# Performance work log

Measured on AMD Instinct MI355X. Metric: run time of the kernel, lower is better.

## Reference

```python
import jax, jax.numpy as jnp
import numpy as np

NEG_INF = -1e9


def setup_inputs() -> dict:
    key = jax.random.key(0)
    ks = jax.random.split(key, 12)
    B, S, D, H = 32, 2048, 512, 512
    enc_outs = jax.random.normal(ks[0], (B, S, D), dtype=jnp.float32)
    num_sent = jnp.maximum(jax.random.randint(ks[1], (B,), 0, S), 1).astype(jnp.int64)
    s = 1.0 / np.sqrt(H)
    return {
        "enc_outs": enc_outs,
        "num_sent": num_sent,
        "num_pred": 8,
        "init_h": jax.random.normal(ks[2], (1, H), dtype=jnp.float32) * s,
        "init_c": jax.random.normal(ks[3], (1, H), dtype=jnp.float32) * s,
        "init_in": jax.random.normal(ks[4], (D,), dtype=jnp.float32) * s,
        "W_ih": jax.random.uniform(ks[5], (4 * H, D), jnp.float32, -s, s),
        "W_hh": jax.random.uniform(ks[6], (4 * H, H), jnp.float32, -s, s),
        "b_ih": jax.random.uniform(ks[7], (4 * H,), jnp.float32, -s, s),
        "b_hh": jax.random.uniform(ks[8], (4 * H,), jnp.float32, -s, s),
        "attn_Wq": jax.random.uniform(ks[9], (H, D), jnp.float32, -s, s),
        "score_W": jax.random.uniform(ks[10], (1, H), jnp.float32, -s, s),
        "score_b": jax.random.uniform(ks[11], (1,), jnp.float32, -s, s),
    }


def reference(enc_outs, num_sent, num_pred, init_h, init_c, init_in,
              W_ih, W_hh, b_ih, b_hh, attn_Wq, score_W, score_b):
    B, S, D = enc_outs.shape
    H = init_h.shape[1]
    # rep_mask: True where sentence index is valid
    mask = jnp.arange(S)[None, :] < num_sent[:, None]  # [B, S]

    def lstm_cell(x, h, c):
        gates = x @ W_ih.T + b_ih + h @ W_hh.T + b_hh  # [B, 4H]
        i, f, g, o = jnp.split(gates, 4, axis=-1)
        i, f, o = jax.nn.sigmoid(i), jax.nn.sigmoid(f), jax.nn.sigmoid(o)
        c_new = f * c + i * jnp.tanh(g)
        return o * jnp.tanh(c_new), c_new

    h0 = jnp.broadcast_to(init_h[0], (B, H))
    c0 = jnp.broadcast_to(init_c[0], (B, H))
    in0 = jnp.broadcast_to(init_in, (B, D))

    def step(carry, _):
        h, c, lstm_in = carry
        h, c = lstm_cell(lstm_in, h, c)
        # glimpse attention: bilinear score, masked softmax over sentences
        q = h @ attn_Wq  # [B, D]
        logits = jnp.einsum('bd,bsd->bs', q, enc_outs)
        logits = jnp.where(mask, logits, NEG_INF)
        attn = jax.nn.softmax(logits, axis=-1)
        out = jnp.einsum('bs,bsd->bd', attn, enc_outs)  # [B, D]
        score = out @ score_W.T + score_b  # [B, 1]
        return (h, c, out), score

    _, scores = jax.lax.scan(step, (h0, c0, in0), None, length=int(num_pred))
    return scores  # [num_pred, B, 1]
```

## Files before the change

### kernel.cpp

```cpp
#include <hip/hip_runtime.h>
#include <math.h>

#define B    32
#define S    2048
#define D    512
#define H    512
#define NP   8
#define NSL  32
#define HSL  16
#define NBT  8
#define BG   4
#define NCH  8
#define SCHUNK 256

__device__ __forceinline__ float sigmoidf_(float x) {
  return 1.0f / (1.0f + __expf(-x));
}

__global__ __launch_bounds__(256)
void k_init(const float* __restrict__ W_ih, const float* __restrict__ W_hh,
            const float* __restrict__ init_h, const float* __restrict__ init_c,
            const float* __restrict__ init_in, const int* __restrict__ ns_raw,
            float* __restrict__ Wt, float* __restrict__ hbuf, float* __restrict__ cbuf,
            float* __restrict__ xin0, int* __restrict__ ns) {
  __shared__ float tbuf[64][65];
  const int blk = blockIdx.x, tid = threadIdx.x;
  const int jt = blk & 31, kt = blk >> 5;
  const int j0 = jt * 64, k0 = kt * 64;
  const int r0 = tid >> 6, cc = tid & 63;
  for (int rr = r0; rr < 64; rr += 4) {
    int j = j0 + rr, k = k0 + cc;
    tbuf[rr][cc] = (k < 512) ? W_ih[(size_t)j * 512 + k]
                             : W_hh[(size_t)j * 512 + (k - 512)];
  }
  __syncthreads();
  for (int rr = r0; rr < 64; rr += 4)
    Wt[(size_t)(k0 + rr) * 2048 + j0 + cc] = tbuf[cc][rr];

  int idx = blk * 256 + tid;
  if (idx < B * H) {
    int d = idx & 511;
    hbuf[idx] = init_h[d];
    cbuf[idx] = init_c[d];
    xin0[idx] = init_in[d];
  }
  if (idx == 0) {
    bool is64 = (ns_raw[1] == 0);
    for (int i = 0; i < B; ++i) ns[i] = is64 ? ns_raw[2 * i] : ns_raw[i];
  }
}

__global__ __launch_bounds__(512, 1)
void k_step(const float* __restrict__ xin0, const float* __restrict__ bih,
            const float* __restrict__ bhh, const float* __restrict__ Wq,
            const float* __restrict__ scW, const float* __restrict__ scb,
            const float* __restrict__ Wt,
            const float* __restrict__ ch_m, const float* __restrict__ ch_l,
            const float* __restrict__ ch_o,
            float* __restrict__ hbuf, float* __restrict__ cbuf,
            float* __restrict__ qpart, float* __restrict__ out, int t) {
  __shared__ float X[BG][1024];
  __shared__ float gacc[8][64][5];
  __shared__ float gl[4][16][BG];
  __shared__ float hl[BG][16];
  __shared__ float sred[8][BG];

  const int tid = threadIdx.x;
  const int sl = blockIdx.x >> 3;
  const int bg = blockIdx.x & 7;
  const int b0 = bg * BG;

  if (t == 0) {
    #pragma unroll
    for (int bl = 0; bl < BG; ++bl)
      X[bl][tid] = xin0[(b0 + bl) * 512 + tid];
  } else {
    const float swd = scW[tid];
    #pragma unroll
    for (int bl = 0; bl < BG; ++bl) {
      const int b = b0 + bl;
      float M = -1e30f;
      #pragma unroll
      for (int c = 0; c < NCH; ++c) M = fmaxf(M, ch_m[b * NCH + c]);
      float e[NCH]; float L = 0.f;
      #pragma unroll
      for (int c = 0; c < NCH; ++c) {
        e[c] = __expf(ch_m[b * NCH + c] - M);
        L += ch_l[b * NCH + c] * e[c];
      }
      float v = 0.f;
      #pragma unroll
      for (int c = 0; c < NCH; ++c)
        v += ch_o[((size_t)(b * NCH + c)) * 512 + tid] * e[c];
      v *= (1.0f / L);
      X[bl][tid] = v;
      float p = v * swd;
      #pragma unroll
      for (int off = 32; off > 0; off >>= 1) p += __shfl_xor(p, off);
      if ((tid & 63) == 0) sred[tid >> 6][bl] = p;
    }
  }
  if (t < NP) {
    const float4* hsrc = (const float4*)(hbuf + (t & 1) * (B * 512));
    int bl = tid >> 7;
    int off = tid & 127;
    float4 hv = hsrc[(b0 + bl) * 128 + off];
    *(float4*)&X[bl][512 + off * 4] = hv;
  }
  __syncthreads();

  if (t >= 1 && tid < BG) {
    float s = 0.f;
    #pragma unroll
    for (int w = 0; w < 8; ++w) s += sred[w][tid];
    if (sl == 0) out[(t - 1) * B + b0 + tid] = s + scb[0];
  }
  if (t >= NP) return;

  {
    const int jloc = tid & 63;
    const int kc = tid >> 6;
    const int gi = jloc >> 4, ho = jloc & 15;
    const int jg = gi * 512 + sl * HSL + ho;
    const int k0c = kc * 128;
    const float* wp = Wt + (size_t)k0c * 2048 + jg;
    float acc[BG] = {0, 0, 0, 0};
    for (int kk = 0; kk < 32; ++kk) {
      float wv0 = wp[(size_t)(kk * 4 + 0) * 2048];
      float wv1 = wp[(size_t)(kk * 4 + 1) * 2048];
      float wv2 = wp[(size_t)(kk * 4 + 2) * 2048];
      float wv3 = wp[(size_t)(kk * 4 + 3) * 2048];
      #pragma unroll
      for (int bl = 0; bl < BG; ++bl) {
        const float4 xv = *(const float4*)&X[bl][k0c + kk * 4];
        acc[bl] += wv0 * xv.x + wv1 * xv.y + wv2 * xv.z + wv3 * xv.w;
      }
    }
    #pragma unroll
    for (int bl = 0; bl < BG; ++bl) gacc[kc][jloc][bl] = acc[bl];
  }
  __syncthreads();

  if (tid < 256) {
    const int bl = tid >> 6, jloc = tid & 63;
    const int gi = jloc >> 4, ho = jloc & 15;
    const int jg = gi * 512 + sl * HSL + ho;
    float g = bih[jg] + bhh[jg];
    #pragma unroll
    for (int kc = 0; kc < 8; ++kc) g += gacc[kc][jloc][bl];
    gl[gi][ho][bl] = g;
  }
  __syncthreads();

  if (tid < BG * HSL) {
    const int ho = tid & 15, bl = tid >> 4;
    const int bglob = b0 + bl, hid = sl * HSL + ho;
    float i_ = sigmoidf_(gl[0][ho][bl]);
    float f_ = sigmoidf_(gl[1][ho][bl]);
    float g_ = tanhf(gl[2][ho][bl]);
    float o_ = sigmoidf_(gl[3][ho][bl]);
    float cv = cbuf[bglob * 512 + hid];
    float cn = f_ * cv + i_ * g_;
    cbuf[bglob * 512 + hid] = cn;
    float hv = o_ * tanhf(cn);
    hbuf[((t + 1) & 1) * (B * 512) + bglob * 512 + hid] = hv;
    hl[bl][ho] = hv;
  }
  __syncthreads();

  {
    float w[HSL];
    #pragma unroll
    for (int ho = 0; ho < HSL; ++ho)
      w[ho] = Wq[(size_t)(sl * HSL + ho) * 512 + tid];
    #pragma unroll
    for (int bl = 0; bl < BG; ++bl) {
      float acc = 0.f;
      #pragma unroll
      for (int ho = 0; ho < HSL; ++ho) acc += hl[bl][ho] * w[ho];
      qpart[((size_t)sl * B + b0 + bl) * 512 + tid] = acc;
    }
  }
}

__global__ __launch_bounds__(512, 1)
void k_attn(const float* __restrict__ enc, const float* __restrict__ qpart,
            const int* __restrict__ ns_buf, float* __restrict__ ch_m,
            float* __restrict__ ch_l, float* __restrict__ ch_o) {
  __shared__ float q_lds[512];
  __shared__ float wm[8], wl[8];
  __shared__ float wo[8][512];
  const int b  = blockIdx.x >> 3;
  const int ch = blockIdx.x & 7;
  const int tid = threadIdx.x;
  const int lane = tid & 63;
  const int wv = tid >> 6;

  {
    float s = 0.f;
    #pragma unroll 8
    for (int sl = 0; sl < NSL; ++sl)
      s += qpart[((size_t)sl * B + b) * 512 + tid];
    q_lds[tid] = s;
  }
  __syncthreads();

  const float4 qa  = *(const float4*)&q_lds[lane * 8];
  const float4 qb4 = *(const float4*)&q_lds[lane * 8 + 4];

  const int s0 = ch * SCHUNK;
  const int nsb = ns_buf[b];
  float m = -1e30f, l = 0.f;
  float o0=0,o1=0,o2=0,o3=0,o4=0,o5=0,o6=0,o7=0;

  const int send = min(s0 + SCHUNK, nsb);
  const size_t rowbase = (size_t)b * S;

  int r = s0 + 2 * wv;
  if (r < send) {
    bool has1 = (r + 1 < send);
    const float4* p0 = (const float4*)(enc + (rowbase + r) * 512 + lane * 8);
    const float4* p1 = (const float4*)(enc + (rowbase + (has1 ? r + 1 : r)) * 512 + lane * 8);
    float4 a0 = p0[0], a1 = p0[1];
    float4 c0 = p1[0], c1 = p1[1];
    while (true) {
      const int rn = r + 16;
      const bool hasn = (rn < send);
      float4 na0, na1, nc0, nc1;
      bool nhas1 = false;
      if (hasn) {
        nhas1 = (rn + 1 < send);
        const float4* f0 = (const float4*)(enc + (rowbase + rn) * 512 + lane * 8);
        const float4* f1 = (const float4*)(enc + (rowbase + (nhas1 ? rn + 1 : rn)) * 512 + lane * 8);
        na0 = f0[0]; na1 = f0[1]; nc0 = f1[0]; nc1 = f1[1];
      }
      float d0 = qa.x*a0.x + qa.y*a0.y + qa.z*a0.z + qa.w*a0.w
               + qb4.x*a1.x + qb4.y*a1.y + qb4.z*a1.z + qb4.w*a1.w;
      float d1 = qa.x*c0.x + qa.y*c0.y + qa.z*c0.z + qa.w*c0.w
               + qb4.x*c1.x + qb4.y*c1.y + qb4.z*c1.z + qb4.w*c1.w;
      #pragma unroll
      for (int off = 32; off > 0; off >>= 1) {
        d0 += __shfl_xor(d0, off);
        d1 += __shfl_xor(d1, off);
      }
      if (!has1) d1 = -1e30f;
      float nm = fmaxf(m, fmaxf(d0, d1));
      float sc = __expf(m - nm);
      float w0 = __expf(d0 - nm);
      float w1 = __expf(d1 - nm);
      l = l * sc + w0 + w1;
      o0 = o0*sc + w0*a0.x + w1*c0.x; o1 = o1*sc + w0*a0.y + w1*c0.y;
      o2 = o2*sc + w0*a0.z + w1*c0.z; o3 = o3*sc + w0*a0.w + w1*c0.w;
      o4 = o4*sc + w0*a1.x + w1*c1.x; o5 = o5*sc + w0*a1.y + w1*c1.y;
      o6 = o6*sc + w0*a1.z + w1*c1.z; o7 = o7*sc + w0*a1.w + w1*c1.w;
      m = nm;
      if (!hasn) break;
      r = rn; has1 = nhas1;
      a0 = na0; a1 = na1; c0 = nc0; c1 = nc1;
    }
  }
  if (lane == 0) { wm[wv] = m; wl[wv] = l; }
  float4* wop = (float4*)&wo[wv][lane * 8];
  wop[0] = make_float4(o0, o1, o2, o3);
  wop[1] = make_float4(o4, o5, o6, o7);
  __syncthreads();

  float M = wm[0];
  #pragma unroll
  for (int w = 1; w < 8; ++w) M = fmaxf(M, wm[w]);
  float e[8]; float L = 0.f;
  #pragma unroll
  for (int w = 0; w < 8; ++w) { e[w] = __expf(wm[w] - M); L += wl[w] * e[w]; }
  if (tid == 0) { ch_m[b * NCH + ch] = M; ch_l[b * NCH + ch] = L; }
  float v = 0.f;
  #pragma unroll
  for (int w = 0; w < 8; ++w) v += wo[w][tid] * e[w];
  ch_o[((size_t)(b * NCH + ch)) * 512 + tid] = v;
}

extern "C" void kernel_launch(void* const* d_in, const int* in_sizes, int n_in,
                              void* d_out, int out_size, void* d_ws, size_t ws_size,
                              hipStream_t stream) {
  const float* enc     = (const float*)d_in[0];
  const int*   ns_raw  = (const int*)d_in[1];
  const float* init_h  = (const float*)d_in[3];
  const float* init_c  = (const float*)d_in[4];
  const float* init_in = (const float*)d_in[5];
  const float* W_ih    = (const float*)d_in[6];
  const float* W_hh    = (const float*)d_in[7];
  const float* b_ih    = (const float*)d_in[8];
  const float* b_hh    = (const float*)d_in[9];
  const float* Wq      = (const float*)d_in[10];
  const float* score_W = (const float*)d_in[11];
  const float* score_b = (const float*)d_in[12];
  float* out = (float*)d_out;

  float* ws    = (float*)d_ws;
  float* Wt    = ws;
  float* hbuf  = ws + 2097152;
  float* cbuf  = ws + 2129920;
  float* xin0  = ws + 2146304;
  float* qpart = ws + 2162688;
  float* ch_m  = ws + 2686976;
  float* ch_l  = ws + 2687232;
  float* ch_o  = ws + 2687488;
  int*   ns    = (int*)(ws + 2818560);

  k_init<<<512, 256, 0, stream>>>(W_ih, W_hh, init_h, init_c, init_in, ns_raw,
                                  Wt, hbuf, cbuf, xin0, ns);
  for (int t = 0; t < NP; ++t) {
    k_step<<<NSL * NBT, 512, 0, stream>>>(xin0, b_ih, b_hh, Wq, score_W, score_b, Wt,
                                          ch_m, ch_l, ch_o, hbuf, cbuf, qpart, out, t);
    k_attn<<<B * NCH, 512, 0, stream>>>(enc, qpart, ns, ch_m, ch_l, ch_o);
  }
  k_step<<<NSL * NBT, 512, 0, stream>>>(xin0, b_ih, b_hh, Wq, score_W, score_b, Wt,
                                        ch_m, ch_l, ch_o, hbuf, cbuf, qpart, out, NP);
}
```

Before: 309.6 us.

## Interleave 8-row groups across all waves to balance attention work per batch

The attention kernel now gives each wave interleaved groups of 8 consecutive sentence rows, strided by 64 groups across all chunk blocks of a batch row. Before, each block owned a fixed 256-row chunk, so for short sequences most blocks sat idle. This spreads the valid rows evenly and raises memory-level parallelism with 8-row double-buffered loads per wave. The cost is heavy register use: 32 float4 buffers per thread may hurt occupancy or spill. The last group may also read up to 7 padded rows past the valid length, which are masked out.

```diff
diff --git a/kernel.cpp b/kernel.cpp
--- a/kernel.cpp
+++ b/kernel.cpp
@@ -208,61 +208,82 @@
   const float4 qa  = *(const float4*)&q_lds[lane * 8];
   const float4 qb4 = *(const float4*)&q_lds[lane * 8 + 4];
 
-  const int s0 = ch * SCHUNK;
   const int nsb = ns_buf[b];
+  const int gid = ch * 8 + wv;
+  const size_t rowbase = (size_t)b * S;
+  const int ngroups = (nsb + 7) >> 3;
+  const int niter = (gid < ngroups) ? ((ngroups - gid + 63) >> 6) : 0;
+
   float m = -1e30f, l = 0.f;
-  float o0=0,o1=0,o2=0,o3=0,o4=0,o5=0,o6=0,o7=0;
-
-  const int send = min(s0 + SCHUNK, nsb);
-  const size_t rowbase = (size_t)b * S;
-
-  int r = s0 + 2 * wv;
-  if (r < send) {
-    bool has1 = (r + 1 < send);
-    const float4* p0 = (const float4*)(enc + (rowbase + r) * 512 + lane * 8);
-    const float4* p1 = (const float4*)(enc + (rowbase + (has1 ? r + 1 : r)) * 512 + lane * 8);
-    float4 a0 = p0[0], a1 = p0[1];
-    float4 c0 = p1[0], c1 = p1[1];
-    while (true) {
-      const int rn = r + 16;
-      const bool hasn = (rn < send);
-      float4 na0, na1, nc0, nc1;
-      bool nhas1 = false;
-      if (hasn) {
-        nhas1 = (rn + 1 < send);
-        const float4* f0 = (const float4*)(enc + (rowbase + rn) * 512 + lane * 8);
-        const float4* f1 = (const float4*)(enc + (rowbase + (nhas1 ? rn + 1 : rn)) * 512 + lane * 8);
-        na0 = f0[0]; na1 = f0[1]; nc0 = f1[0]; nc1 = f1[1];
-      }
-      float d0 = qa.x*a0.x + qa.y*a0.y + qa.z*a0.z + qa.w*a0.w
-               + qb4.x*a1.x + qb4.y*a1.y + qb4.z*a1.z + qb4.w*a1.w;
-      float d1 = qa.x*c0.x + qa.y*c0.y + qa.z*c0.z + qa.w*c0.w
-               + qb4.x*c1.x + qb4.y*c1.y + qb4.z*c1.z + qb4.w*c1.w;
+  float4 acc0 = make_float4(0,0,0,0), acc1 = make_float4(0,0,0,0);
+
+  float4 cx[8], cy[8], nx[8], ny[8];
+
+#define LOADG(g, X, Y)                                                        \
+  {                                                                           \
+    const size_t rb = rowbase + (size_t)(g) * 8;                              \
+    _Pragma("unroll")                                                         \
+    for (int j = 0; j < 8; ++j) {                                             \
+      const float4* p = (const float4*)(enc + (rb + j) * 512 + lane * 8);     \
+      X[j] = p[0]; Y[j] = p[1];                                               \
+    }                                                                         \
+  }
+
+  if (niter > 0) {
+    int g = gid;
+    LOADG(g, cx, cy);
+    for (int i = 0; i < niter; ++i) {
+      const bool has = (i + 1 < niter);
+      if (has) LOADG(g + 64, nx, ny);
+
+      float d[8];
+      #pragma unroll
+      for (int j = 0; j < 8; ++j)
+        d[j] = qa.x*cx[j].x + qa.y*cx[j].y + qa.z*cx[j].z + qa.w*cx[j].w
+             + qb4.x*cy[j].x + qb4.y*cy[j].y + qb4.z*cy[j].z + qb4.w*cy[j].w;
       #pragma unroll
       for (int off = 32; off > 0; off >>= 1) {
-        d0 += __shfl_xor(d0, off);
-        d1 += __shfl_xor(d1, off);
-      }
-      if (!has1) d1 = -1e30f;
-      float nm = fmaxf(m, fmaxf(d0, d1));
+        #pragma unroll
+        for (int j = 0; j < 8; ++j) d[j] += __shfl_xor(d[j], off);
+      }
+      const int rbase = g * 8;
+      #pragma unroll
+      for (int j = 0; j < 8; ++j)
+        if (rbase + j >= nsb) d[j] = -1e30f;
+
+      float gm = fmaxf(fmaxf(fmaxf(d[0], d[1]), fmaxf(d[2], d[3])),
+                       fmaxf(fmaxf(d[4], d[5]), fmaxf(d[6], d[7])));
+      float nm = fmaxf(m, gm);
       float sc = __expf(m - nm);
-      float w0 = __expf(d0 - nm);
-      float w1 = __expf(d1 - nm);
-      l = l * sc + w0 + w1;
-      o0 = o0*sc + w0*a0.x + w1*c0.x; o1 = o1*sc + w0*a0.y + w1*c0.y;
-      o2 = o2*sc + w0*a0.z + w1*c0.z; o3 = o3*sc + w0*a0.w + w1*c0.w;
-      o4 = o4*sc + w0*a1.x + w1*c1.x; o5 = o5*sc + w0*a1.y + w1*c1.y;
-      o6 = o6*sc + w0*a1.z + w1*c1.z; o7 = o7*sc + w0*a1.w + w1*c1.w;
+      float w[8];
+      float ws = 0.f;
+      #pragma unroll
+      for (int j = 0; j < 8; ++j) { w[j] = __expf(d[j] - nm); ws += w[j]; }
+      l = l * sc + ws;
+      acc0.x *= sc; acc0.y *= sc; acc0.z *= sc; acc0.w *= sc;
+      acc1.x *= sc; acc1.y *= sc; acc1.z *= sc; acc1.w *= sc;
+      #pragma unroll
+      for (int j = 0; j < 8; ++j) {
+        acc0.x += w[j] * cx[j].x; acc0.y += w[j] * cx[j].y;
+        acc0.z += w[j] * cx[j].z; acc0.w += w[j] * cx[j].w;
+        acc1.x += w[j] * cy[j].x; acc1.y += w[j] * cy[j].y;
+        acc1.z += w[j] * cy[j].z; acc1.w += w[j] * cy[j].w;
+      }
       m = nm;
-      if (!hasn) break;
-      r = rn; has1 = nhas1;
-      a0 = na0; a1 = na1; c0 = nc0; c1 = nc1;
+
+      if (has) {
+        #pragma unroll
+        for (int j = 0; j < 8; ++j) { cx[j] = nx[j]; cy[j] = ny[j]; }
+        g += 64;
+      }
     }
   }
+#undef LOADG
+
   if (lane == 0) { wm[wv] = m; wl[wv] = l; }
   float4* wop = (float4*)&wo[wv][lane * 8];
-  wop[0] = make_float4(o0, o1, o2, o3);
-  wop[1] = make_float4(o4, o5, o6, o7);
+  wop[0] = acc0;
+  wop[1] = acc1;
   __syncthreads();
 
   float M = wm[0];
```

After: 327.2 us. 1.06x slower.
